# Optimization experiments

Hardware: AMD Instinct MI355X
Metric: run time of the kernel (lower is better)

Reference implementation:

```python
import jax, jax.numpy as jnp
import numpy as np

EPS = 1e-12
FP8_MAX = 448.0  # torch.finfo(float8_e4m3fn).max
G = 128  # tile/block group size


def per_tile_quant_dequant(x):
    # x: [seq, din]; one scale per 1x128 tile along din (per_tile_quant semantics)
    s, d = x.shape
    xt = x.reshape(s, d // G, G)
    amax = jnp.max(jnp.abs(xt), axis=-1, keepdims=True)
    scale = jnp.maximum(amax, EPS) / FP8_MAX
    q = jnp.clip(xt / scale, -FP8_MAX, FP8_MAX).astype(jnp.float8_e4m3fn)
    return (q.astype(jnp.float32) * scale).reshape(s, d)


def per_block_quant_dequant(w):
    # w: [ne, dout, din]; one scale per 128x128 block
    ne, dout, din = w.shape
    wb = w.reshape(ne, dout // G, G, din // G, G)
    amax = jnp.max(jnp.abs(wb), axis=(2, 4), keepdims=True)
    scale = jnp.maximum(amax, EPS) / FP8_MAX
    q = jnp.clip(wb / scale, -FP8_MAX, FP8_MAX).astype(jnp.float8_e4m3fn)
    return (q.astype(jnp.float32) * scale).reshape(ne, dout, din)


def grouped_gemm(xq, wq, tokens_per_expert):
    # xq: [seq, din] (tokens contiguous per expert); wq: [ne, dout, din]
    seq = xq.shape[0]
    ne, dout, _ = wq.shape
    ends = jnp.cumsum(tokens_per_expert)
    starts = ends - tokens_per_expert
    tok = jnp.arange(seq)
    out = jnp.zeros((seq, dout), dtype=jnp.float32)
    for e in range(ne):  # small fixed expert count
        mask = ((tok >= starts[e]) & (tok < ends[e]))[:, None]
        xe = jnp.where(mask, xq, 0.0)
        out = out + xe @ wq[e].T
    return out


def setup_inputs() -> dict:
    key = jax.random.key(0)
    k1, k2 = jax.random.split(key)
    ne, dout, din, seq = 8, 2048, 2048, 8192
    x = jax.random.normal(k1, (seq, din), dtype=jnp.float32)
    # weight stored flat as (ne*dout, din), as in the module
    weight = jax.random.normal(k2, (ne * dout, din), dtype=jnp.float32) * 0.02
    tokens_per_expert = jnp.full((ne,), seq // ne, dtype=jnp.int32)
    return {"input": x, "weight": weight, "tokens_per_expert": tokens_per_expert}


def reference(input, weight, tokens_per_expert):
    ne, dout, din = 8, 2048, 2048
    w = weight.reshape(ne, dout, din)
    xq = per_tile_quant_dequant(input)          # per-tile fp8 activation quant
    wq = per_block_quant_dequant(w)             # per-block fp8 weight quant
    return grouped_gemm(xq, wq, tokens_per_expert)
```

## Files before the change

### kernel.cpp

```cpp
#include <hip/hip_runtime.h>
#include <hip/hip_bf16.h>
#include <stdint.h>

#define NE   8
#define DOUT 2048
#define DIN  2048
#define SEQ  8192
#define GSZ  128
#define FP8_MAX 448.0f
#define EPSQ 1e-12f

typedef float f32x4  __attribute__((ext_vector_type(4)));
typedef float f32x16 __attribute__((ext_vector_type(16)));
typedef int   i32x4  __attribute__((ext_vector_type(4)));
typedef int   i32x8  __attribute__((ext_vector_type(8)));

__device__ __forceinline__ void async16(void* lds_base, const void* gptr) {
    __builtin_amdgcn_global_load_lds(
        (const __attribute__((address_space(1))) unsigned int*)gptr,
        (__attribute__((address_space(3))) unsigned int*)lds_base,
        16, 0, 0);
}

__global__ __launch_bounds__(256) void quant_x_kernel(
    const float* __restrict__ x, unsigned char* __restrict__ qx,
    float* __restrict__ sx)
{
    const int g = blockIdx.x * 256 + threadIdx.x;
    const float4 v = ((const float4*)x)[g];
    float a = fmaxf(fmaxf(fabsf(v.x), fabsf(v.y)),
                    fmaxf(fabsf(v.z), fabsf(v.w)));
    #pragma unroll
    for (int o = 16; o; o >>= 1) a = fmaxf(a, __shfl_xor(a, o));
    const float scale = fmaxf(a, EPSQ) / FP8_MAX;
    const int tile = g >> 5;
    if ((threadIdx.x & 31) == 0) sx[tile] = scale;

    float q0 = fminf(fmaxf(v.x / scale, -FP8_MAX), FP8_MAX);
    float q1 = fminf(fmaxf(v.y / scale, -FP8_MAX), FP8_MAX);
    float q2 = fminf(fmaxf(v.z / scale, -FP8_MAX), FP8_MAX);
    float q3 = fminf(fmaxf(v.w / scale, -FP8_MAX), FP8_MAX);
    int lo = __builtin_amdgcn_cvt_pk_fp8_f32(q0, q1, 0, false);
    int pk = __builtin_amdgcn_cvt_pk_fp8_f32(q2, q3, lo, true);
    ((unsigned int*)qx)[g] = (unsigned int)pk;
}

__global__ __launch_bounds__(256) void quant_w_kernel(
    const float* __restrict__ w, unsigned char* __restrict__ qw,
    float* __restrict__ sw)
{
    __shared__ float buf[128 * 128];
    __shared__ float red[4];

    const int cb = blockIdx.x;
    const int rb = blockIdx.y;
    const int e  = blockIdx.z;
    const int t  = threadIdx.x;
    const int lane = t & 63, wv = t >> 6;

    const size_t base = ((size_t)e * DOUT + rb * GSZ) * DIN + cb * GSZ;
    const float* wp = w + base;

    #pragma unroll
    for (int j = 0; j < 16; ++j) {
        int f16 = (wv * 16 + j) * 64 + lane;
        int row = f16 >> 5, cc = f16 & 31;
        async16(buf + (wv * 16 + j) * 256,
                wp + (size_t)row * DIN + cc * 4);
    }
    __syncthreads();

    float a = 0.f;
    #pragma unroll
    for (int i = 0; i < 16; ++i) {
        f32x4 v = *(const f32x4*)(buf + (t + i * 256) * 4);
        a = fmaxf(a, fmaxf(fmaxf(fabsf(v[0]), fabsf(v[1])),
                           fmaxf(fabsf(v[2]), fabsf(v[3]))));
    }
    #pragma unroll
    for (int o = 32; o; o >>= 1) a = fmaxf(a, __shfl_xor(a, o));
    if (lane == 0) red[wv] = a;
    __syncthreads();
    a = fmaxf(fmaxf(red[0], red[1]), fmaxf(red[2], red[3]));
    const float scale = fmaxf(a, EPSQ) / FP8_MAX;
    if (t == 0) sw[(e * 16 + rb) * 16 + cb] = scale;

    unsigned int* qout = (unsigned int*)(qw + base);
    #pragma unroll
    for (int i = 0; i < 16; ++i) {
        int idx = t + i * 256;
        f32x4 v = *(const f32x4*)(buf + idx * 4);
        float q0 = fminf(fmaxf(v[0] / scale, -FP8_MAX), FP8_MAX);
        float q1 = fminf(fmaxf(v[1] / scale, -FP8_MAX), FP8_MAX);
        float q2 = fminf(fmaxf(v[2] / scale, -FP8_MAX), FP8_MAX);
        float q3 = fminf(fmaxf(v[3] / scale, -FP8_MAX), FP8_MAX);
        int lo = __builtin_amdgcn_cvt_pk_fp8_f32(q0, q1, 0, false);
        int pk = __builtin_amdgcn_cvt_pk_fp8_f32(q2, q3, lo, true);
        int r = idx >> 5, c4 = idx & 31;
        qout[r * (DIN / 4) + c4] = (unsigned int)pk;
    }
}

__global__ __launch_bounds__(512, 2) void gemm_kernel(
    const unsigned char* __restrict__ qx, const float* __restrict__ sx,
    const unsigned char* __restrict__ qw, const float* __restrict__ sw,
    const int* __restrict__ tpe, float* __restrict__ out)
{
    __shared__ __align__(16) unsigned char Asm[2][256 * 128];
    __shared__ __align__(16) unsigned char Bsm[2][256 * 128];
    __shared__ __align__(16) float Rs[16 * 256];
    __shared__ __align__(16) float SwL[2 * 16];

    const int tid  = threadIdx.x;
    const int lane = tid & 63;
    const int wv   = tid >> 6;
    const int wm   = wv >> 2;
    const int wn   = wv & 3;
    const int l31  = lane & 31;
    const int h    = lane >> 5;
    const int nh   = wn >> 1;

    const int lid  = blockIdx.x;
    const int xcd  = lid & 7, t8 = lid >> 3;
    const int mbid = xcd * 4 + (t8 >> 3);
    const int nb   = t8 & 7;
    const int r0   = mbid * 256, n0 = nb * 256;

    int e = -1, start = 0;
    #pragma unroll
    for (int i = 0; i < NE; ++i) {
        int end = start + tpe[i];
        if (r0 >= start && r0 < end) e = i;
        start = end;
    }
    if (e < 0) {
        f32x4 z = {0.f, 0.f, 0.f, 0.f};
        for (int i = tid; i < 256 * 64; i += 512) {
            int r = i >> 6, c4 = i & 63;
            *(f32x4*)(out + (size_t)(r0 + r) * DOUT + n0 + c4 * 4) = z;
        }
        return;
    }

    for (int i = tid; i < 16 * 256; i += 512) {
        int row = i >> 4, kb = i & 15;
        const float* sp = sx + (size_t)(r0 + row) * 16;
        Rs[kb * 256 + row] = (kb == 0) ? sp[15] : sp[kb - 1] / sp[kb];
    }
    if (tid < 32) {
        int nhh = tid >> 4, kb = tid & 15;
        const float* wp = sw + ((e * 16) + (nb * 2 + nhh)) * 16;
        SwL[nhh * 16 + kb] = (kb == 0) ? wp[15] : wp[kb - 1] / wp[kb];
    }

    const unsigned char* Ag = qx + (size_t)r0 * DIN;
    const unsigned char* Bg = qw + (size_t)e * DOUT * DIN + (size_t)n0 * DIN;

    int soff[4], ldst[4];
    #pragma unroll
    for (int j = 0; j < 4; ++j) {
        int f = wv * 4096 + j * 1024 + lane * 16;
        int row = f >> 7, pc = (f >> 4) & 7;
        soff[j] = row * DIN + ((pc ^ (row & 7)) * 16);
        ldst[j] = wv * 4096 + j * 1024;
    }

    int abase[4], ax8[4], bbase[2], bx8[2];
    #pragma unroll
    for (int mi = 0; mi < 4; ++mi) {
        int ra = wm * 128 + mi * 32 + l31;
        abase[mi] = ra * 128; ax8[mi] = ra & 7;
    }
    #pragma unroll
    for (int ni = 0; ni < 2; ++ni) {
        int rb = wn * 64 + ni * 32 + l31;
        bbase[ni] = rb * 128; bx8[ni] = rb & 7;
    }

    #pragma unroll
    for (int j = 0; j < 4; ++j) {
        async16(Asm[0] + ldst[j], Ag + soff[j]);
        async16(Bsm[0] + ldst[j], Bg + soff[j]);
    }
    asm volatile("s_waitcnt lgkmcnt(0)" ::: "memory");

    f32x16 acc[4][2];
    #pragma unroll
    for (int mi = 0; mi < 4; ++mi)
        #pragma unroll
        for (int ni = 0; ni < 2; ++ni)
            #pragma unroll
            for (int q = 0; q < 16; ++q) acc[mi][ni][q] = 0.f;

    for (int kb = 0; kb < 16; ++kb) {
        const unsigned char* Ac = Asm[kb & 1];
        const unsigned char* Bc = Bsm[kb & 1];

        if (kb < 15) {
            unsigned char* An = Asm[(kb & 1) ^ 1];
            unsigned char* Bn = Bsm[(kb & 1) ^ 1];
            #pragma unroll
            for (int j = 0; j < 4; ++j) {
                async16(An + ldst[j], Ag + soff[j] + (kb + 1) * GSZ);
                async16(Bn + ldst[j], Bg + soff[j] + (kb + 1) * GSZ);
            }
            asm volatile("s_waitcnt vmcnt(8)" ::: "memory");
        } else {
            asm volatile("s_waitcnt vmcnt(0)" ::: "memory");
        }
        __builtin_amdgcn_s_barrier();
        asm volatile("" ::: "memory");

        if (kb) {
            const float rwk = SwL[nh * 16 + kb];
            #pragma unroll
            for (int mi = 0; mi < 4; ++mi) {
                const float* rp = Rs + kb * 256 + wm * 128 + mi * 32 + 4 * h;
                f32x4 rr[4];
                #pragma unroll
                for (int g = 0; g < 4; ++g) {
                    f32x4 t = *(const f32x4*)(rp + 8 * g);
                    rr[g] = t * rwk;
                }
                #pragma unroll
                for (int ni = 0; ni < 2; ++ni)
                    #pragma unroll
                    for (int g = 0; g < 4; ++g)
                        #pragma unroll
                        for (int j = 0; j < 4; ++j)
                            acc[mi][ni][g * 4 + j] *= rr[g][j];
            }
        }

        __builtin_amdgcn_s_setprio(1);
        #pragma unroll
        for (int ks = 0; ks < 2; ++ks) {
            const int c0 = ks * 4 + h * 2;
            i32x8 Bf[2];
            #pragma unroll
            for (int ni = 0; ni < 2; ++ni) {
                i32x4 lo = *(const i32x4*)(Bc + bbase[ni] + (((c0    ) ^ bx8[ni]) * 16));
                i32x4 hi = *(const i32x4*)(Bc + bbase[ni] + (((c0 + 1) ^ bx8[ni]) * 16));
                #pragma unroll
                for (int q = 0; q < 4; ++q) { Bf[ni][q] = lo[q]; Bf[ni][q + 4] = hi[q]; }
            }
            #pragma unroll
            for (int mi = 0; mi < 4; ++mi) {
                i32x8 Af;
                i32x4 alo = *(const i32x4*)(Ac + abase[mi] + (((c0    ) ^ ax8[mi]) * 16));
                i32x4 ahi = *(const i32x4*)(Ac + abase[mi] + (((c0 + 1) ^ ax8[mi]) * 16));
                #pragma unroll
                for (int q = 0; q < 4; ++q) { Af[q] = alo[q]; Af[q + 4] = ahi[q]; }
                #pragma unroll
                for (int ni = 0; ni < 2; ++ni)
                    acc[mi][ni] = __builtin_amdgcn_mfma_scale_f32_32x32x64_f8f6f4(
                        Af, Bf[ni], acc[mi][ni],
                        0, 0,
                        0, 0x7f7f7f7f,
                        0, 0x7f7f7f7f);
            }
        }
        __builtin_amdgcn_s_setprio(0);
        asm volatile("" ::: "memory");
        __builtin_amdgcn_s_barrier();
        asm volatile("" ::: "memory");
    }

    const float fw = SwL[nh * 16 + 0];
    #pragma unroll
    for (int mi = 0; mi < 4; ++mi) {
        const float* fp = Rs + wm * 128 + mi * 32 + 4 * h;
        f32x4 fv[4];
        #pragma unroll
        for (int g = 0; g < 4; ++g) {
            f32x4 t = *(const f32x4*)(fp + 8 * g);
            fv[g] = t * fw;
        }
        const int rbase = r0 + wm * 128 + mi * 32 + 4 * h;
        #pragma unroll
        for (int ni = 0; ni < 2; ++ni) {
            const int col = n0 + wn * 64 + ni * 32 + l31;
            #pragma unroll
            for (int g = 0; g < 4; ++g)
                #pragma unroll
                for (int j = 0; j < 4; ++j)
                    out[(size_t)(rbase + 8 * g + j) * DOUT + col] =
                        acc[mi][ni][g * 4 + j] * fv[g][j];
        }
    }
}

extern "C" void kernel_launch(void* const* d_in, const int* in_sizes, int n_in,
                              void* d_out, int out_size, void* d_ws, size_t ws_size,
                              hipStream_t stream) {
    const float* x   = (const float*)d_in[0];
    const float* wt  = (const float*)d_in[1];
    const int*   tpe = (const int*)d_in[2];
    float* out = (float*)d_out;

    char* ws = (char*)d_ws;
    unsigned char* qx = (unsigned char*)ws;
    unsigned char* qw = qx + (size_t)SEQ * DIN;
    float* sx = (float*)(qw + (size_t)NE * DOUT * DIN);
    float* sw = sx + (size_t)SEQ * 16;

    quant_x_kernel<<<SEQ * DIN / 4 / 256, 256, 0, stream>>>(x, qx, sx);
    quant_w_kernel<<<dim3(16, 16, NE), 256, 0, stream>>>(wt, qw, sw);
    gemm_kernel<<<256, 512, 0, stream>>>(qx, sx, qw, sw, tpe, out);
}
```

Measured before the change: 302.4 us.

## Split K-step into two halves and stagger A/B prefetch around mid barrier

Each 128-wide K step now runs as two 64-wide MFMA halves separated by an extra barrier. The next stage's A tile is prefetched before the first half and its B tile after the mid barrier, so the wait only covers the A loads. The per-block scale rescale moves after the MFMAs and uses the next block's ratio, with the final block applying the first-block factor, which removes the epilogue scaling. The aim is to spread memory traffic across the step and overlap it with compute, at the cost of one extra barrier per step and less lead time for the B loads.

```diff
diff --git a/kernel.cpp b/kernel.cpp
--- a/kernel.cpp
+++ b/kernel.cpp
@@ -195,27 +195,92 @@
     for (int kb = 0; kb < 16; ++kb) {
         const unsigned char* Ac = Asm[kb & 1];
         const unsigned char* Bc = Bsm[kb & 1];
+        unsigned char* An = Asm[(kb & 1) ^ 1];
+        unsigned char* Bn = Bsm[(kb & 1) ^ 1];
 
         if (kb < 15) {
-            unsigned char* An = Asm[(kb & 1) ^ 1];
-            unsigned char* Bn = Bsm[(kb & 1) ^ 1];
-            #pragma unroll
-            for (int j = 0; j < 4; ++j) {
+            #pragma unroll
+            for (int j = 0; j < 4; ++j)
                 async16(An + ldst[j], Ag + soff[j] + (kb + 1) * GSZ);
-                async16(Bn + ldst[j], Bg + soff[j] + (kb + 1) * GSZ);
-            }
-            asm volatile("s_waitcnt vmcnt(8)" ::: "memory");
+            asm volatile("s_waitcnt vmcnt(4)" ::: "memory");
         } else {
             asm volatile("s_waitcnt vmcnt(0)" ::: "memory");
         }
         __builtin_amdgcn_s_barrier();
         asm volatile("" ::: "memory");
 
-        if (kb) {
-            const float rwk = SwL[nh * 16 + kb];
+        {
+            const int c0 = h * 2;
+            i32x8 Bk[2];
+            #pragma unroll
+            for (int ni = 0; ni < 2; ++ni) {
+                i32x4 lo = *(const i32x4*)(Bc + bbase[ni] + (((c0    ) ^ bx8[ni]) * 16));
+                i32x4 hi = *(const i32x4*)(Bc + bbase[ni] + (((c0 + 1) ^ bx8[ni]) * 16));
+                #pragma unroll
+                for (int q = 0; q < 4; ++q) { Bk[ni][q] = lo[q]; Bk[ni][q + 4] = hi[q]; }
+            }
+            i32x8 Afr[4];
             #pragma unroll
             for (int mi = 0; mi < 4; ++mi) {
-                const float* rp = Rs + kb * 256 + wm * 128 + mi * 32 + 4 * h;
+                i32x4 lo = *(const i32x4*)(Ac + abase[mi] + (((c0    ) ^ ax8[mi]) * 16));
+                i32x4 hi = *(const i32x4*)(Ac + abase[mi] + (((c0 + 1) ^ ax8[mi]) * 16));
+                #pragma unroll
+                for (int q = 0; q < 4; ++q) { Afr[mi][q] = lo[q]; Afr[mi][q + 4] = hi[q]; }
+            }
+            __builtin_amdgcn_s_setprio(1);
+            #pragma unroll
+            for (int mi = 0; mi < 4; ++mi)
+                #pragma unroll
+                for (int ni = 0; ni < 2; ++ni)
+                    acc[mi][ni] = __builtin_amdgcn_mfma_scale_f32_32x32x64_f8f6f4(
+                        Afr[mi], Bk[ni], acc[mi][ni],
+                        0, 0, 0, 0x7f7f7f7f, 0, 0x7f7f7f7f);
+            __builtin_amdgcn_s_setprio(0);
+        }
+        asm volatile("" ::: "memory");
+        __builtin_amdgcn_s_barrier();
+        asm volatile("" ::: "memory");
+
+        if (kb < 15) {
+            #pragma unroll
+            for (int j = 0; j < 4; ++j)
+                async16(Bn + ldst[j], Bg + soff[j] + (kb + 1) * GSZ);
+        }
+        {
+            const int c0 = 4 + h * 2;
+            i32x8 Bk[2];
+            #pragma unroll
+            for (int ni = 0; ni < 2; ++ni) {
+                i32x4 lo = *(const i32x4*)(Bc + bbase[ni] + (((c0    ) ^ bx8[ni]) * 16));
+                i32x4 hi = *(const i32x4*)(Bc + bbase[ni] + (((c0 + 1) ^ bx8[ni]) * 16));
+                #pragma unroll
+                for (int q = 0; q < 4; ++q) { Bk[ni][q] = lo[q]; Bk[ni][q + 4] = hi[q]; }
+            }
+            i32x8 Afr[4];
+            #pragma unroll
+            for (int mi = 0; mi < 4; ++mi) {
+                i32x4 lo = *(const i32x4*)(Ac + abase[mi] + (((c0    ) ^ ax8[mi]) * 16));
+                i32x4 hi = *(const i32x4*)(Ac + abase[mi] + (((c0 + 1) ^ ax8[mi]) * 16));
+                #pragma unroll
+                for (int q = 0; q < 4; ++q) { Afr[mi][q] = lo[q]; Afr[mi][q + 4] = hi[q]; }
+            }
+            __builtin_amdgcn_s_setprio(1);
+            #pragma unroll
+            for (int mi = 0; mi < 4; ++mi)
+                #pragma unroll
+                for (int ni = 0; ni < 2; ++ni)
+                    acc[mi][ni] = __builtin_amdgcn_mfma_scale_f32_32x32x64_f8f6f4(
+                        Afr[mi], Bk[ni], acc[mi][ni],
+                        0, 0, 0, 0x7f7f7f7f, 0, 0x7f7f7f7f);
+            __builtin_amdgcn_s_setprio(0);
+        }
+
+        {
+            const int kk = (kb < 15) ? kb + 1 : 0;
+            const float rwk = SwL[nh * 16 + kk];
+            #pragma unroll
+            for (int mi = 0; mi < 4; ++mi) {
+                const float* rp = Rs + kk * 256 + wm * 128 + mi * 32 + 4 * h;
                 f32x4 rr[4];
                 #pragma unroll
                 for (int g = 0; g < 4; ++g) {
@@ -231,51 +296,13 @@
                             acc[mi][ni][g * 4 + j] *= rr[g][j];
             }
         }
-
-        __builtin_amdgcn_s_setprio(1);
-        #pragma unroll
-        for (int ks = 0; ks < 2; ++ks) {
-            const int c0 = ks * 4 + h * 2;
-            i32x8 Bf[2];
-            #pragma unroll
-            for (int ni = 0; ni < 2; ++ni) {
-                i32x4 lo = *(const i32x4*)(Bc + bbase[ni] + (((c0    ) ^ bx8[ni]) * 16));
-                i32x4 hi = *(const i32x4*)(Bc + bbase[ni] + (((c0 + 1) ^ bx8[ni]) * 16));
-                #pragma unroll
-                for (int q = 0; q < 4; ++q) { Bf[ni][q] = lo[q]; Bf[ni][q + 4] = hi[q]; }
-            }
-            #pragma unroll
-            for (int mi = 0; mi < 4; ++mi) {
-                i32x8 Af;
-                i32x4 alo = *(const i32x4*)(Ac + abase[mi] + (((c0    ) ^ ax8[mi]) * 16));
-                i32x4 ahi = *(const i32x4*)(Ac + abase[mi] + (((c0 + 1) ^ ax8[mi]) * 16));
-                #pragma unroll
-                for (int q = 0; q < 4; ++q) { Af[q] = alo[q]; Af[q + 4] = ahi[q]; }
-                #pragma unroll
-                for (int ni = 0; ni < 2; ++ni)
-                    acc[mi][ni] = __builtin_amdgcn_mfma_scale_f32_32x32x64_f8f6f4(
-                        Af, Bf[ni], acc[mi][ni],
-                        0, 0,
-                        0, 0x7f7f7f7f,
-                        0, 0x7f7f7f7f);
-            }
-        }
-        __builtin_amdgcn_s_setprio(0);
         asm volatile("" ::: "memory");
         __builtin_amdgcn_s_barrier();
         asm volatile("" ::: "memory");
     }
 
-    const float fw = SwL[nh * 16 + 0];
     #pragma unroll
     for (int mi = 0; mi < 4; ++mi) {
-        const float* fp = Rs + wm * 128 + mi * 32 + 4 * h;
-        f32x4 fv[4];
-        #pragma unroll
-        for (int g = 0; g < 4; ++g) {
-            f32x4 t = *(const f32x4*)(fp + 8 * g);
-            fv[g] = t * fw;
-        }
         const int rbase = r0 + wm * 128 + mi * 32 + 4 * h;
         #pragma unroll
         for (int ni = 0; ni < 2; ++ni) {
@@ -285,7 +312,7 @@
                 #pragma unroll
                 for (int j = 0; j < 4; ++j)
                     out[(size_t)(rbase + 8 * g + j) * DOUT + col] =
-                        acc[mi][ni][g * 4 + j] * fv[g][j];
+                        acc[mi][ni][g * 4 + j];
         }
     }
 }
```

Measured after the change: 307.8 us. Within noise of the previous version (+1.8%).
